# Kernel optimization log

Measured on AMD Instinct MI355X. Metric: run time of the kernel, lower is better.

The kernel has to match this reference:

```python
import jax, jax.numpy as jnp
import numpy as np
from jax import lax

N_NODES = 20000
DEG = 32  # fixed out-degree so per-node edge lists reshape to [N, DEG]


def qmul(q, r):
    # Hamilton product, last dim = (w, x, y, z)
    w1, x1, y1, z1 = q[..., 0], q[..., 1], q[..., 2], q[..., 3]
    w2, x2, y2, z2 = r[..., 0], r[..., 1], r[..., 2], r[..., 3]
    return jnp.stack([
        w1 * w2 - x1 * x2 - y1 * y2 - z1 * z2,
        w1 * x2 + x1 * w2 + y1 * z2 - z1 * y2,
        w1 * y2 - x1 * z2 + y1 * w2 + z1 * x2,
        w1 * z2 + x1 * y2 - y1 * x2 + z1 * w2,
    ], axis=-1)


def inv_q(q):
    # conjugate == inverse for unit quaternions
    return q * jnp.array([1.0, -1.0, -1.0, -1.0], dtype=q.dtype)


def quaternion2deg(q):
    # rotation angle in degrees: 2*acos(|w|)
    w = jnp.clip(jnp.abs(q[..., 0]), 0.0, 1.0)
    return 2.0 * jnp.degrees(jnp.arccos(w))


def setup_inputs() -> dict:
    key = jax.random.key(0)
    k1, k2 = jax.random.split(key)
    E = N_NODES * DEG
    src = jnp.repeat(jnp.arange(N_NODES, dtype=jnp.int32), DEG)
    dst = jax.random.randint(k1, (E,), 0, N_NODES, dtype=jnp.int32)
    edge_index = jnp.stack([src, dst], axis=0)  # [2, E]
    q = jax.random.normal(k2, (E, 4), dtype=jnp.float32)
    edge_attr = q / jnp.linalg.norm(q, axis=-1, keepdims=True)  # unit quats
    return {"edge_attr": edge_attr, "edge_index": edge_index, "start_node": 0}


def _bfs_spt(edge_attr, edge_index, start_node):
    src, dst = edge_index[0], edge_index[1]
    N = int(jnp.max(edge_index)) + 1          # node_num (eager, concrete)
    E = edge_attr.shape[0]
    deg = E // N                               # fixed out-degree

    # per-source-node sort of outgoing edges by rotation error (ascending)
    err = quaternion2deg(edge_attr)
    order = jnp.lexsort((err, src))            # primary key src, secondary err
    nbr = dst[order].reshape(N, deg)           # [N, DEG] destination nodes
    nbr_q = edge_attr[order].reshape(N, deg, 4)  # [N, DEG, 4] edge quats

    queue0 = jnp.zeros((N,), jnp.int32).at[0].set(jnp.int32(start_node))
    visited0 = jnp.zeros((N,), bool).at[start_node].set(True)
    quat0 = jnp.zeros((N, 4), edge_attr.dtype).at[:, 0].set(1.0)  # identity

    def outer(carry, head):
        queue, tail, visited, nq = carry
        u = queue[head]
        active = head < tail                   # queue not yet exhausted
        qu = nq[u]                             # u's quat is final by BFS order

        def inner(c, xs):
            queue, tail, visited, nq = c
            v, q = xs
            take = active & (~visited[v])
            qn = qmul(inv_q(q), qu)
            nq = nq.at[v].set(jnp.where(take, qn, nq[v]))
            # when tail == N all nodes are enqueued so take is False and the
            # clamped OOB write is a harmless self-assignment
            queue = queue.at[tail].set(jnp.where(take, v, queue[tail]))
            visited = visited.at[v].set(visited[v] | take)
            tail = tail + take.astype(jnp.int32)
            return (queue, tail, visited, nq), None

        carry, _ = lax.scan(inner, (queue, tail, visited, nq), (nbr[u], nbr_q[u]))
        return carry, None

    init = (queue0, jnp.int32(1), visited0, quat0)
    (queue, tail, visited, node_quat), _ = lax.scan(outer, init, jnp.arange(N))
    return node_quat


def reference(edge_attr, edge_index, start_node):
    node_quat = _bfs_spt(edge_attr, edge_index, start_node)
    return (start_node, node_quat)
```

## Files before the change

kernel.cpp:

```cpp
#include <hip/hip_runtime.h>

constexpr int DEG = 32;
constexpr int BLOCKS = 64;
constexpr int THREADS = 256;
constexpr int SOLO_MAX = 64;

__global__ void sort_edges_kernel(const float* __restrict__ eattr,
                                  const int* __restrict__ dst,
                                  int* __restrict__ nbr,
                                  int* __restrict__ eidx,
                                  unsigned* __restrict__ bar,
                                  int E) {
    if (blockIdx.x == 0 && threadIdx.x < 2) bar[threadIdx.x] = 0u;
    __shared__ float serr[256];
    int e = blockIdx.x * 256 + threadIdx.x;
    float err = 1e30f;
    if (e < E) {
        float w = fabsf(eattr[e * 4 + 0]);
        w = fminf(w, 1.0f);
        float a = acosf(w);
        err = 2.0f * (a * 57.29577951308232f);
    }
    serr[threadIdx.x] = err;
    __syncthreads();
    if (e < E) {
        int s = e & (DEG - 1);
        int base = (int)threadIdx.x - s;
        int rank = 0;
        for (int t = 0; t < DEG; ++t) {
            float et = serr[base + t];
            rank += (int)((et < err) || (et == err && t < s));
        }
        int u = e >> 5;
        nbr[(u << 5) + rank] = dst[e];
        eidx[(u << 5) + rank] = e;
    }
}

__device__ __forceinline__ int ld_ag(const int* p) {
    return __hip_atomic_load(p, __ATOMIC_RELAXED, __HIP_MEMORY_SCOPE_AGENT);
}
__device__ __forceinline__ void st_ag(int* p, int v) {
    __hip_atomic_store(p, v, __ATOMIC_RELAXED, __HIP_MEMORY_SCOPE_AGENT);
}
__device__ __forceinline__ float ldf_ag(const float* p) {
    return __int_as_float(ld_ag((const int*)p));
}
__device__ __forceinline__ void stf_ag(float* p, float v) {
    st_ag((int*)p, __float_as_int(v));
}

__device__ __forceinline__ void gsync(unsigned* bar, unsigned& phase) {
    __syncthreads();
    if (threadIdx.x == 0) {
        phase += 1u;
        unsigned target = phase * (unsigned)BLOCKS;
        unsigned old = __hip_atomic_fetch_add(&bar[0], 1u, __ATOMIC_RELAXED,
                                              __HIP_MEMORY_SCOPE_AGENT);
        if (old + 1u == target) {
            __hip_atomic_store(&bar[1], phase, __ATOMIC_RELAXED,
                               __HIP_MEMORY_SCOPE_AGENT);
        } else {
            while (__hip_atomic_load(&bar[1], __ATOMIC_RELAXED,
                                     __HIP_MEMORY_SCOPE_AGENT) < phase)
                __builtin_amdgcn_s_sleep(2);
        }
    }
    __syncthreads();
}

__global__ void __launch_bounds__(THREADS)
bfs_kernel(const float* __restrict__ eattr,
           const int* __restrict__ nbr,
           const int* __restrict__ eidx,
           int* __restrict__ queue,
           int* __restrict__ claim,
           unsigned* __restrict__ state,
           int* __restrict__ ctrl,
           unsigned* __restrict__ bar,
           float* __restrict__ out,
           const int* __restrict__ startp,
           int N) {
    const int tid = blockIdx.x * blockDim.x + threadIdx.x;
    const int T = gridDim.x * blockDim.x;
    float* quat = out + 1;
    const float4* eattr4 = (const float4*)eattr;
    const int start = *startp;
    unsigned phase = 0;

    __shared__ int s_wsum[THREADS / 64];
    __shared__ int s_wbase[THREADS / 64];
    __shared__ int s_carry;
    __shared__ int s_excl;
    __shared__ int s_total;

    for (int v = tid; v < N; v += T) {
        st_ag(&claim[v], (v == start) ? -1 : 0x7FFFFFFF);
        stf_ag(&quat[4 * v + 0], 1.0f);
        stf_ag(&quat[4 * v + 1], 0.0f);
        stf_ag(&quat[4 * v + 2], 0.0f);
        stf_ag(&quat[4 * v + 3], 0.0f);
    }
    if (tid == 0) {
        st_ag(&queue[0], start);
        out[0] = (float)start;
    }
    gsync(bar, phase);

    int head = 0, tail = 1;
    unsigned gen = 0;
    while (head < tail) {
        const int F = tail - head;

        if (F <= SOLO_MAX) {
            if (blockIdx.x == 0) {
                int h = head, t = tail;
                while (h < t && (t - h) <= SOLO_MAX) {
                    const int Fb = t - h;
                    for (int e = threadIdx.x; e < Fb * DEG; e += THREADS) {
                        int p = h + (e >> 5), s = e & 31;
                        int u = ld_ag(&queue[p]);
                        int v = nbr[(u << 5) + s];
                        atomicMin(&claim[v], (p << 5) + s);
                    }
                    __syncthreads();
                    int my_c = 0;
                    if ((int)threadIdx.x < Fb) {
                        int p = h + (int)threadIdx.x, u = ld_ag(&queue[p]);
                        for (int s = 0; s < DEG; ++s) {
                            int v = nbr[(u << 5) + s];
                            if (ld_ag(&claim[v]) == ((p << 5) + s)) my_c++;
                        }
                    }
                    int incl = my_c;
                    for (int d = 1; d < 64; d <<= 1) {
                        int tt = __shfl_up(incl, d, 64);
                        if ((threadIdx.x & 63) >= (unsigned)d) incl += tt;
                    }
                    if (threadIdx.x == 63) s_total = incl;
                    __syncthreads();
                    int total = s_total;
                    if ((int)threadIdx.x < Fb) {
                        int p = h + (int)threadIdx.x, u = ld_ag(&queue[p]);
                        int pos = t + (incl - my_c);
                        float pw = ldf_ag(&quat[4 * u + 0]);
                        float px = ldf_ag(&quat[4 * u + 1]);
                        float py = ldf_ag(&quat[4 * u + 2]);
                        float pz = ldf_ag(&quat[4 * u + 3]);
                        for (int s = 0; s < DEG; ++s) {
                            int v = nbr[(u << 5) + s];
                            if (ld_ag(&claim[v]) == ((p << 5) + s)) {
                                float4 q = eattr4[eidx[(u << 5) + s]];
                                float qw = q.x, qx = -q.y, qy = -q.z, qz = -q.w;
                                stf_ag(&quat[4 * v + 0], qw * pw - qx * px - qy * py - qz * pz);
                                stf_ag(&quat[4 * v + 1], qw * px + qx * pw + qy * pz - qz * py);
                                stf_ag(&quat[4 * v + 2], qw * py - qx * pz + qy * pw + qz * px);
                                stf_ag(&quat[4 * v + 3], qw * pz + qx * py - qy * px + qz * pw);
                                st_ag(&queue[pos++], v);
                            }
                        }
                    }
                    __syncthreads();
                    h = t;
                    t += total;
                }
                if (threadIdx.x == 0) { st_ag(&ctrl[1], h); st_ag(&ctrl[2], t); }
            }
            gsync(bar, phase);
            head = ld_ag(&ctrl[1]);
            tail = ld_ag(&ctrl[2]);
        } else {
            {
                const int EDG = F * DEG;
                for (int e = tid; e < EDG; e += 4 * T) {
                    int ee[4]; bool ok[4]; int u[4], v[4];
                    #pragma unroll
                    for (int k = 0; k < 4; ++k) {
                        ee[k] = e + k * T;
                        ok[k] = ee[k] < EDG;
                        u[k] = ok[k] ? ld_ag(&queue[head + (ee[k] >> 5)]) : 0;
                    }
                    #pragma unroll
                    for (int k = 0; k < 4; ++k)
                        v[k] = ok[k] ? nbr[(u[k] << 5) + (ee[k] & 31)] : 0;
                    #pragma unroll
                    for (int k = 0; k < 4; ++k)
                        if (ok[k])
                            atomicMin(&claim[v[k]],
                                      ((head + (ee[k] >> 5)) << 5) + (ee[k] & 31));
                }
            }
            gsync(bar, phase);

            gen++;
            const int CH = (F + BLOCKS - 1) / BLOCKS;
            const int c0 = blockIdx.x * CH;
            const int c1 = min(F, c0 + CH);
            if (threadIdx.x == 0) s_carry = 0;
            __syncthreads();

            int ms[2] = {0, 0}, ofs[2] = {0, 0};
            #pragma unroll
            for (int st = 0; st < 2; ++st) {
                int i = c0 + st * THREADS + (int)threadIdx.x;
                int x = 0, mask = 0;
                if (i < c1) {
                    int p = head + i, u = ld_ag(&queue[p]);
                    const int4* row = (const int4*)&nbr[u << 5];
                    int vv[32];
                    #pragma unroll
                    for (int r = 0; r < 8; ++r) {
                        int4 q4 = row[r];
                        vv[4 * r + 0] = q4.x; vv[4 * r + 1] = q4.y;
                        vv[4 * r + 2] = q4.z; vv[4 * r + 3] = q4.w;
                    }
                    int cl[32];
                    #pragma unroll
                    for (int s = 0; s < 32; ++s) cl[s] = ld_ag(&claim[vv[s]]);
                    #pragma unroll
                    for (int s = 0; s < 32; ++s)
                        if (cl[s] == ((p << 5) + s)) { mask |= 1 << s; x++; }
                }
                int lane = threadIdx.x & 63, wid = threadIdx.x >> 6;
                int incl = x;
                for (int d = 1; d < 64; d <<= 1) {
                    int tt = __shfl_up(incl, d, 64);
                    if (lane >= d) incl += tt;
                }
                if (lane == 63) s_wsum[wid] = incl;
                __syncthreads();
                if (threadIdx.x == 0) {
                    int acc = s_carry;
                    for (int w = 0; w < THREADS / 64; ++w) {
                        s_wbase[w] = acc;
                        acc += s_wsum[w];
                    }
                    s_carry = acc;
                }
                __syncthreads();
                ms[st] = mask;
                ofs[st] = s_wbase[wid] + incl - x;
                __syncthreads();
            }
            const int agg = s_carry;

            if (threadIdx.x == 0)
                __hip_atomic_store(&state[blockIdx.x],
                                   ((gen & 0xFFu) << 24) | (unsigned)agg,
                                   __ATOMIC_RELAXED, __HIP_MEMORY_SCOPE_AGENT);
            if (threadIdx.x < 64) {
                unsigned sv;
                do {
                    sv = __hip_atomic_load(&state[threadIdx.x], __ATOMIC_RELAXED,
                                           __HIP_MEMORY_SCOPE_AGENT);
                } while ((sv >> 24) != (gen & 0xFFu));
                int a = (int)(sv & 0xFFFFFFu);
                int incl = a;
                for (int d = 1; d < 64; d <<= 1) {
                    int tt = __shfl_up(incl, d, 64);
                    if ((int)(threadIdx.x & 63) >= d) incl += tt;
                }
                int myincl = __shfl(incl, (int)blockIdx.x, 64);
                int mya = __shfl(a, (int)blockIdx.x, 64);
                int tot = __shfl(incl, 63, 64);
                if (threadIdx.x == 0) { s_excl = myincl - mya; s_total = tot; }
            }
            __syncthreads();
            const int excl = s_excl;
            const int total = s_total;

            #pragma unroll
            for (int st = 0; st < 2; ++st) {
                int i = c0 + st * THREADS + (int)threadIdx.x;
                int mask = ms[st];
                if (i < c1 && mask) {
                    int p = head + i, u = ld_ag(&queue[p]);
                    int pos = tail + excl + ofs[st];
                    float pw = ldf_ag(&quat[4 * u + 0]);
                    float px = ldf_ag(&quat[4 * u + 1]);
                    float py = ldf_ag(&quat[4 * u + 2]);
                    float pz = ldf_ag(&quat[4 * u + 3]);
                    while (mask) {
                        int s = __ffs(mask) - 1;
                        mask &= mask - 1;
                        int v = nbr[(u << 5) + s];
                        float4 q = eattr4[eidx[(u << 5) + s]];
                        float qw = q.x, qx = -q.y, qy = -q.z, qz = -q.w;
                        stf_ag(&quat[4 * v + 0], qw * pw - qx * px - qy * py - qz * pz);
                        stf_ag(&quat[4 * v + 1], qw * px + qx * pw + qy * pz - qz * py);
                        stf_ag(&quat[4 * v + 2], qw * py - qx * pz + qy * pw + qz * px);
                        stf_ag(&quat[4 * v + 3], qw * pz + qx * py - qy * px + qz * pw);
                        st_ag(&queue[pos++], v);
                    }
                }
            }
            gsync(bar, phase);
            head = tail;
            tail += total;
        }
    }
}

extern "C" void kernel_launch(void* const* d_in, const int* in_sizes, int n_in,
                              void* d_out, int out_size, void* d_ws, size_t ws_size,
                              hipStream_t stream) {
    const float* eattr = (const float*)d_in[0];
    const int* edge_index = (const int*)d_in[1];
    const int* startp = (const int*)d_in[2];
    const int E = in_sizes[0] / 4;
    const int N = E / DEG;
    const int* dst = edge_index + E;

    char* ws = (char*)d_ws;
    int* nbr = (int*)ws;            ws += (size_t)E * 4;
    int* eidx = (int*)ws;           ws += (size_t)E * 4;
    int* queue = (int*)ws;          ws += (size_t)N * 4;
    int* claim = (int*)ws;          ws += (size_t)N * 4;
    unsigned int* state = (unsigned int*)ws; ws += (size_t)BLOCKS * 4;
    int* ctrl = (int*)ws;           ws += 64;
    unsigned int* bar = (unsigned int*)ws; ws += 64;

    sort_edges_kernel<<<dim3((E + 255) / 256), dim3(256), 0, stream>>>(
        eattr, dst, nbr, eidx, bar, E);

    float* out = (float*)d_out;
    void* args[] = {(void*)&eattr, (void*)&nbr,   (void*)&eidx, (void*)&queue,
                    (void*)&claim, (void*)&state, (void*)&ctrl, (void*)&bar,
                    (void*)&out,   (void*)&startp, (void*)&N};
    (void)hipLaunchCooperativeKernel((void*)bfs_kernel, dim3(BLOCKS),
                                     dim3(THREADS), args, 0, stream);
}
```

Before: 278.4 us.

## Carry parent quaternions in queue records and use per-block flag barrier

Queue entries become 32-byte records holding the node id and its quaternion, so expanding a frontier node reads its parent rotation from the record instead of gathering from the output array. Output quaternion writes become plain stores, and the identity fill moves to a final pass over unreached nodes. The claim step now checks the current value before issuing atomicMin, and the grid barrier changes from a shared atomic counter to per-block phase flags polled by one wavefront. This trades an 8x larger queue footprint and extra loads for fewer atomics and shorter barrier latency.

```diff
diff --git a/kernel.cpp b/kernel.cpp
--- a/kernel.cpp
+++ b/kernel.cpp
@@ -1,4 +1,6 @@
 #include <hip/hip_runtime.h>
+
+typedef unsigned long long ull;
 
 constexpr int DEG = 32;
 constexpr int BLOCKS = 64;
@@ -9,9 +11,9 @@
                                   const int* __restrict__ dst,
                                   int* __restrict__ nbr,
                                   int* __restrict__ eidx,
-                                  unsigned* __restrict__ bar,
+                                  unsigned* __restrict__ slot,
                                   int E) {
-    if (blockIdx.x == 0 && threadIdx.x < 2) bar[threadIdx.x] = 0u;
+    if (blockIdx.x == 0 && threadIdx.x < 64) slot[threadIdx.x] = 0u;
     __shared__ float serr[256];
     int e = blockIdx.x * 256 + threadIdx.x;
     float err = 1e30f;
@@ -43,28 +45,23 @@
 __device__ __forceinline__ void st_ag(int* p, int v) {
     __hip_atomic_store(p, v, __ATOMIC_RELAXED, __HIP_MEMORY_SCOPE_AGENT);
 }
-__device__ __forceinline__ float ldf_ag(const float* p) {
-    return __int_as_float(ld_ag((const int*)p));
-}
-__device__ __forceinline__ void stf_ag(float* p, float v) {
-    st_ag((int*)p, __float_as_int(v));
-}
-
-__device__ __forceinline__ void gsync(unsigned* bar, unsigned& phase) {
+__device__ __forceinline__ ull ld8(const ull* p) {
+    return __hip_atomic_load(p, __ATOMIC_RELAXED, __HIP_MEMORY_SCOPE_AGENT);
+}
+__device__ __forceinline__ void st8(ull* p, ull v) {
+    __hip_atomic_store(p, v, __ATOMIC_RELAXED, __HIP_MEMORY_SCOPE_AGENT);
+}
+
+__device__ __forceinline__ void gsync(unsigned* slot, unsigned& phase) {
     __syncthreads();
-    if (threadIdx.x == 0) {
-        phase += 1u;
-        unsigned target = phase * (unsigned)BLOCKS;
-        unsigned old = __hip_atomic_fetch_add(&bar[0], 1u, __ATOMIC_RELAXED,
-                                              __HIP_MEMORY_SCOPE_AGENT);
-        if (old + 1u == target) {
-            __hip_atomic_store(&bar[1], phase, __ATOMIC_RELAXED,
-                               __HIP_MEMORY_SCOPE_AGENT);
-        } else {
-            while (__hip_atomic_load(&bar[1], __ATOMIC_RELAXED,
-                                     __HIP_MEMORY_SCOPE_AGENT) < phase)
-                __builtin_amdgcn_s_sleep(2);
-        }
+    ++phase;
+    if (threadIdx.x == 0)
+        __hip_atomic_store(&slot[blockIdx.x], phase, __ATOMIC_RELAXED,
+                           __HIP_MEMORY_SCOPE_AGENT);
+    if (threadIdx.x < 64) {
+        while (__hip_atomic_load(&slot[threadIdx.x], __ATOMIC_RELAXED,
+                                 __HIP_MEMORY_SCOPE_AGENT) < phase)
+            __builtin_amdgcn_s_sleep(1);
     }
     __syncthreads();
 }
@@ -73,11 +70,11 @@
 bfs_kernel(const float* __restrict__ eattr,
            const int* __restrict__ nbr,
            const int* __restrict__ eidx,
-           int* __restrict__ queue,
+           ull* __restrict__ qrec,
            int* __restrict__ claim,
            unsigned* __restrict__ state,
            int* __restrict__ ctrl,
-           unsigned* __restrict__ bar,
+           unsigned* __restrict__ slot,
            float* __restrict__ out,
            const int* __restrict__ startp,
            int N) {
@@ -94,18 +91,21 @@
     __shared__ int s_excl;
     __shared__ int s_total;
 
-    for (int v = tid; v < N; v += T) {
-        st_ag(&claim[v], (v == start) ? -1 : 0x7FFFFFFF);
-        stf_ag(&quat[4 * v + 0], 1.0f);
-        stf_ag(&quat[4 * v + 1], 0.0f);
-        stf_ag(&quat[4 * v + 2], 0.0f);
-        stf_ag(&quat[4 * v + 3], 0.0f);
-    }
+    for (int i = tid; i < (N >> 1); i += T) {
+        int v0 = 2 * i, v1 = 2 * i + 1;
+        unsigned lo = (v0 == start) ? 0xFFFFFFFFu : 0x7FFFFFFFu;
+        unsigned hi = (v1 == start) ? 0xFFFFFFFFu : 0x7FFFFFFFu;
+        st8(&((ull*)claim)[i], (ull)lo | ((ull)hi << 32));
+    }
+    if ((N & 1) && tid == 0)
+        st_ag(&claim[N - 1], (N - 1 == start) ? -1 : 0x7FFFFFFF);
     if (tid == 0) {
-        st_ag(&queue[0], start);
+        st8(&qrec[0], (ull)(unsigned)start | ((ull)0x3F800000u << 32));
+        st8(&qrec[1], 0ull);
+        st8(&qrec[2], 0ull);
         out[0] = (float)start;
     }
-    gsync(bar, phase);
+    gsync(slot, phase);
 
     int head = 0, tail = 1;
     unsigned gen = 0;
@@ -119,18 +119,19 @@
                     const int Fb = t - h;
                     for (int e = threadIdx.x; e < Fb * DEG; e += THREADS) {
                         int p = h + (e >> 5), s = e & 31;
-                        int u = ld_ag(&queue[p]);
+                        int u = (int)(unsigned)ld8(&qrec[4 * p]);
                         int v = nbr[(u << 5) + s];
-                        atomicMin(&claim[v], (p << 5) + s);
+                        int key = (p << 5) + s;
+                        if (ld_ag(&claim[v]) > key) atomicMin(&claim[v], key);
                     }
                     __syncthreads();
                     int my_c = 0;
                     if ((int)threadIdx.x < Fb) {
-                        int p = h + (int)threadIdx.x, u = ld_ag(&queue[p]);
-                        for (int s = 0; s < DEG; ++s) {
-                            int v = nbr[(u << 5) + s];
-                            if (ld_ag(&claim[v]) == ((p << 5) + s)) my_c++;
-                        }
+                        int p = h + (int)threadIdx.x;
+                        int u = (int)(unsigned)ld8(&qrec[4 * p]);
+                        for (int s = 0; s < DEG; ++s)
+                            if (ld_ag(&claim[nbr[(u << 5) + s]]) == ((p << 5) + s))
+                                my_c++;
                     }
                     int incl = my_c;
                     for (int d = 1; d < 64; d <<= 1) {
@@ -141,22 +142,35 @@
                     __syncthreads();
                     int total = s_total;
                     if ((int)threadIdx.x < Fb) {
-                        int p = h + (int)threadIdx.x, u = ld_ag(&queue[p]);
+                        int p = h + (int)threadIdx.x;
+                        ull r0 = ld8(&qrec[4 * p]);
+                        ull r1 = ld8(&qrec[4 * p + 1]);
+                        ull r2 = ld8(&qrec[4 * p + 2]);
+                        int u = (int)(unsigned)r0;
+                        float pw = __uint_as_float((unsigned)(r0 >> 32));
+                        float px = __uint_as_float((unsigned)r1);
+                        float py = __uint_as_float((unsigned)(r1 >> 32));
+                        float pz = __uint_as_float((unsigned)r2);
                         int pos = t + (incl - my_c);
-                        float pw = ldf_ag(&quat[4 * u + 0]);
-                        float px = ldf_ag(&quat[4 * u + 1]);
-                        float py = ldf_ag(&quat[4 * u + 2]);
-                        float pz = ldf_ag(&quat[4 * u + 3]);
                         for (int s = 0; s < DEG; ++s) {
                             int v = nbr[(u << 5) + s];
                             if (ld_ag(&claim[v]) == ((p << 5) + s)) {
                                 float4 q = eattr4[eidx[(u << 5) + s]];
                                 float qw = q.x, qx = -q.y, qy = -q.z, qz = -q.w;
-                                stf_ag(&quat[4 * v + 0], qw * pw - qx * px - qy * py - qz * pz);
-                                stf_ag(&quat[4 * v + 1], qw * px + qx * pw + qy * pz - qz * py);
-                                stf_ag(&quat[4 * v + 2], qw * py - qx * pz + qy * pw + qz * px);
-                                stf_ag(&quat[4 * v + 3], qw * pz + qx * py - qy * px + qz * pw);
-                                st_ag(&queue[pos++], v);
+                                float nw = qw * pw - qx * px - qy * py - qz * pz;
+                                float nx = qw * px + qx * pw + qy * pz - qz * py;
+                                float ny = qw * py - qx * pz + qy * pw + qz * px;
+                                float nz = qw * pz + qx * py - qy * px + qz * pw;
+                                quat[4 * v + 0] = nw;
+                                quat[4 * v + 1] = nx;
+                                quat[4 * v + 2] = ny;
+                                quat[4 * v + 3] = nz;
+                                st8(&qrec[4 * pos],
+                                    (ull)(unsigned)v | ((ull)__float_as_uint(nw) << 32));
+                                st8(&qrec[4 * pos + 1],
+                                    (ull)__float_as_uint(nx) | ((ull)__float_as_uint(ny) << 32));
+                                st8(&qrec[4 * pos + 2], (ull)__float_as_uint(nz));
+                                pos++;
                             }
                         }
                     }
@@ -166,31 +180,34 @@
                 }
                 if (threadIdx.x == 0) { st_ag(&ctrl[1], h); st_ag(&ctrl[2], t); }
             }
-            gsync(bar, phase);
+            gsync(slot, phase);
             head = ld_ag(&ctrl[1]);
             tail = ld_ag(&ctrl[2]);
         } else {
             {
                 const int EDG = F * DEG;
                 for (int e = tid; e < EDG; e += 4 * T) {
-                    int ee[4]; bool ok[4]; int u[4], v[4];
+                    int ee[4]; bool ok[4]; int u[4], v[4], key[4], cl[4];
                     #pragma unroll
                     for (int k = 0; k < 4; ++k) {
                         ee[k] = e + k * T;
                         ok[k] = ee[k] < EDG;
-                        u[k] = ok[k] ? ld_ag(&queue[head + (ee[k] >> 5)]) : 0;
+                        int p = head + (ee[k] >> 5);
+                        key[k] = (p << 5) + (ee[k] & 31);
+                        u[k] = ok[k] ? (int)(unsigned)ld8(&qrec[4 * p]) : 0;
                     }
                     #pragma unroll
                     for (int k = 0; k < 4; ++k)
                         v[k] = ok[k] ? nbr[(u[k] << 5) + (ee[k] & 31)] : 0;
                     #pragma unroll
                     for (int k = 0; k < 4; ++k)
-                        if (ok[k])
-                            atomicMin(&claim[v[k]],
-                                      ((head + (ee[k] >> 5)) << 5) + (ee[k] & 31));
-                }
-            }
-            gsync(bar, phase);
+                        cl[k] = ok[k] ? ld_ag(&claim[v[k]]) : -1;
+                    #pragma unroll
+                    for (int k = 0; k < 4; ++k)
+                        if (ok[k] && cl[k] > key[k]) atomicMin(&claim[v[k]], key[k]);
+                }
+            }
+            gsync(slot, phase);
 
             gen++;
             const int CH = (F + BLOCKS - 1) / BLOCKS;
@@ -205,7 +222,8 @@
                 int i = c0 + st * THREADS + (int)threadIdx.x;
                 int x = 0, mask = 0;
                 if (i < c1) {
-                    int p = head + i, u = ld_ag(&queue[p]);
+                    int p = head + i;
+                    int u = (int)(unsigned)ld8(&qrec[4 * p]);
                     const int4* row = (const int4*)&nbr[u << 5];
                     int vv[32];
                     #pragma unroll
@@ -274,29 +292,52 @@
                 int i = c0 + st * THREADS + (int)threadIdx.x;
                 int mask = ms[st];
                 if (i < c1 && mask) {
-                    int p = head + i, u = ld_ag(&queue[p]);
+                    int p = head + i;
+                    ull r0 = ld8(&qrec[4 * p]);
+                    ull r1 = ld8(&qrec[4 * p + 1]);
+                    ull r2 = ld8(&qrec[4 * p + 2]);
+                    int u = (int)(unsigned)r0;
+                    float pw = __uint_as_float((unsigned)(r0 >> 32));
+                    float px = __uint_as_float((unsigned)r1);
+                    float py = __uint_as_float((unsigned)(r1 >> 32));
+                    float pz = __uint_as_float((unsigned)r2);
                     int pos = tail + excl + ofs[st];
-                    float pw = ldf_ag(&quat[4 * u + 0]);
-                    float px = ldf_ag(&quat[4 * u + 1]);
-                    float py = ldf_ag(&quat[4 * u + 2]);
-                    float pz = ldf_ag(&quat[4 * u + 3]);
                     while (mask) {
                         int s = __ffs(mask) - 1;
                         mask &= mask - 1;
                         int v = nbr[(u << 5) + s];
                         float4 q = eattr4[eidx[(u << 5) + s]];
                         float qw = q.x, qx = -q.y, qy = -q.z, qz = -q.w;
-                        stf_ag(&quat[4 * v + 0], qw * pw - qx * px - qy * py - qz * pz);
-                        stf_ag(&quat[4 * v + 1], qw * px + qx * pw + qy * pz - qz * py);
-                        stf_ag(&quat[4 * v + 2], qw * py - qx * pz + qy * pw + qz * px);
-                        stf_ag(&quat[4 * v + 3], qw * pz + qx * py - qy * px + qz * pw);
-                        st_ag(&queue[pos++], v);
-                    }
-                }
-            }
-            gsync(bar, phase);
+                        float nw = qw * pw - qx * px - qy * py - qz * pz;
+                        float nx = qw * px + qx * pw + qy * pz - qz * py;
+                        float ny = qw * py - qx * pz + qy * pw + qz * px;
+                        float nz = qw * pz + qx * py - qy * px + qz * pw;
+                        quat[4 * v + 0] = nw;
+                        quat[4 * v + 1] = nx;
+                        quat[4 * v + 2] = ny;
+                        quat[4 * v + 3] = nz;
+                        st8(&qrec[4 * pos],
+                            (ull)(unsigned)v | ((ull)__float_as_uint(nw) << 32));
+                        st8(&qrec[4 * pos + 1],
+                            (ull)__float_as_uint(nx) | ((ull)__float_as_uint(ny) << 32));
+                        st8(&qrec[4 * pos + 2], (ull)__float_as_uint(nz));
+                        pos++;
+                    }
+                }
+            }
+            gsync(slot, phase);
             head = tail;
             tail += total;
+        }
+    }
+
+    for (int v = tid; v < N; v += T) {
+        int c = ld_ag(&claim[v]);
+        if (c == 0x7FFFFFFF || c == -1) {
+            quat[4 * v + 0] = 1.0f;
+            quat[4 * v + 1] = 0.0f;
+            quat[4 * v + 2] = 0.0f;
+            quat[4 * v + 3] = 0.0f;
         }
     }
 }
@@ -314,18 +355,18 @@
     char* ws = (char*)d_ws;
     int* nbr = (int*)ws;            ws += (size_t)E * 4;
     int* eidx = (int*)ws;           ws += (size_t)E * 4;
-    int* queue = (int*)ws;          ws += (size_t)N * 4;
+    ull* qrec = (ull*)ws;           ws += (size_t)N * 32;
     int* claim = (int*)ws;          ws += (size_t)N * 4;
     unsigned int* state = (unsigned int*)ws; ws += (size_t)BLOCKS * 4;
     int* ctrl = (int*)ws;           ws += 64;
-    unsigned int* bar = (unsigned int*)ws; ws += 64;
+    unsigned int* slot = (unsigned int*)ws; ws += 256;
 
     sort_edges_kernel<<<dim3((E + 255) / 256), dim3(256), 0, stream>>>(
-        eattr, dst, nbr, eidx, bar, E);
+        eattr, dst, nbr, eidx, slot, E);
 
     float* out = (float*)d_out;
-    void* args[] = {(void*)&eattr, (void*)&nbr,   (void*)&eidx, (void*)&queue,
-                    (void*)&claim, (void*)&state, (void*)&ctrl, (void*)&bar,
+    void* args[] = {(void*)&eattr, (void*)&nbr,   (void*)&eidx, (void*)&qrec,
+                    (void*)&claim, (void*)&state, (void*)&ctrl, (void*)&slot,
                     (void*)&out,   (void*)&startp, (void*)&N};
     (void)hipLaunchCooperativeKernel((void*)bfs_kernel, dim3(BLOCKS),
                                      dim3(THREADS), args, 0, stream);
```

After: 262.7 us. 1.06x faster.
